# Performance work log

Measured on AMD Instinct MI355X. Metric: run time of the kernel, lower is better.

The kernel has to match this reference:

```python
import jax, jax.numpy as jnp
import numpy as np

N = 1048576          # total points
B = 2048             # number of point clouds (segments)
FEAT = 64            # per-point feature dim
ENC = 32             # neighborhood encoder output dim
RADIUS = 1.0


def _linear_params(key, fan_in, fan_out):
    k1, k2 = jax.random.split(key)
    bound = 1.0 / np.sqrt(fan_in)
    w = jax.random.uniform(k1, (fan_in, fan_out), minval=-bound, maxval=bound, dtype=jnp.float32)
    b = jax.random.uniform(k2, (fan_out,), minval=-bound, maxval=bound, dtype=jnp.float32)
    return w, b


def setup_inputs() -> dict:
    key = jax.random.key(0)
    ks = jax.random.split(key, 10)
    points = jax.random.normal(ks[0], (N, 3), dtype=jnp.float32)
    features = jax.random.normal(ks[1], (N, FEAT), dtype=jnp.float32)
    batch = jnp.sort(jax.random.randint(ks[2], (N,), 0, B)).astype(jnp.int64)
    w_ne, b_ne = _linear_params(ks[3], 3, ENC)
    w1, b1 = _linear_params(ks[4], ENC + FEAT, 128)
    w2, b2 = _linear_params(ks[5], 128, 128)
    w3, b3 = _linear_params(ks[6], 128, 128)
    wg1, bg1 = _linear_params(ks[7], 128, 128)
    wg2, bg2 = _linear_params(ks[8], 128, 64)
    wg3, bg3 = _linear_params(ks[9], 64, 32)
    return {"points": points, "features": features, "batch": batch,
            "w_ne": w_ne, "b_ne": b_ne,
            "w1": w1, "b1": b1, "w2": w2, "b2": b2, "w3": w3, "b3": b3,
            "wg1": wg1, "bg1": bg1, "wg2": wg2, "bg2": bg2, "wg3": wg3, "bg3": bg3}


def _segment_max(x, batch, num_segments):
    pooled = jax.ops.segment_max(x, batch, num_segments=num_segments, indices_are_sorted=True)
    # guard empty segments (segment_max fills with -inf)
    return jnp.where(jnp.isneginf(pooled), 0.0, pooled)


def reference(points, features, batch, w_ne, b_ne, w1, b1, w2, b2, w3, b3,
              wg1, bg1, wg2, bg2, wg3, bg3):
    relative_points = points / RADIUS                       # [N, 3]
    # neighborhood encoder: per-point Linear+ReLU, then segment max-pool -> [B, ENC]
    enc = jax.nn.relu(relative_points @ w_ne + b_ne)        # [N, ENC]
    rel_encoded = _segment_max(enc, batch, B)               # [B, ENC]
    rel_enc_mapped = rel_encoded[batch]                     # gather -> [N, ENC]
    fc_input = jnp.concatenate([rel_enc_mapped, features], axis=1)  # [N, ENC+FEAT]
    h = jax.nn.relu(fc_input @ w1 + b1)                     # [N, 128]
    h = jax.nn.relu(h @ w2 + b2)                            # [N, 128]
    h = jax.nn.relu(h @ w3 + b3)                            # [N, 128]
    pooled = _segment_max(h, batch, B)                      # [B, 128]
    g = jax.nn.relu(pooled @ wg1 + bg1)                     # [B, 128]
    g = jax.nn.relu(g @ wg2 + bg2)                          # [B, 64]
    g = jax.nn.relu(g @ wg3 + bg3)                          # [B, 32]
    return g
```

## Files before the change

### kernel.cpp

```cpp
#include <hip/hip_runtime.h>
#include <hip/hip_fp16.h>

#define N_PTS 1048576
#define BSEG  2048
#define XSTR  72

typedef _Float16 half8  __attribute__((ext_vector_type(8)));
typedef _Float16 half4  __attribute__((ext_vector_type(4)));
typedef _Float16 half2v __attribute__((ext_vector_type(2)));
typedef float    floatx4 __attribute__((ext_vector_type(4)));

__global__ __launch_bounds__(256) void wconv(const float* __restrict__ w1,
                                             const float* __restrict__ w2,
                                             const float* __restrict__ w3,
                                             _Float16* __restrict__ w1T,
                                             _Float16* __restrict__ w2T,
                                             _Float16* __restrict__ w3T) {
    int idx = blockIdx.x * 256 + threadIdx.x;
    if (idx < 8192) {
        int j = idx >> 6, k = idx & 63;
        w1T[idx] = (_Float16)w1[(32 + k) * 128 + j];
    } else if (idx < 8192 + 16384) {
        int i = idx - 8192; int j = i >> 7, k = i & 127;
        w2T[i] = (_Float16)w2[k * 128 + j];
    } else if (idx < 8192 + 32768) {
        int i = idx - 8192 - 16384; int j = i >> 7, k = i & 127;
        w3T[i] = (_Float16)w3[k * 128 + j];
    }
}

__global__ __launch_bounds__(256) void enc_pool(const float* __restrict__ pts,
                                                const int* __restrict__ batch,
                                                const float* __restrict__ wne,
                                                const float* __restrict__ bne,
                                                const float* __restrict__ w1,
                                                const float* __restrict__ b1,
                                                float* __restrict__ b1p) {
    const int b = blockIdx.x, tid = threadIdx.x;
    __shared__ float swne[96];
    __shared__ float sbne[32];
    __shared__ float red[4][32];
    __shared__ float sEnc[32];
    if (tid < 96) swne[tid] = wne[tid];
    if (tid < 32) sbne[tid] = bne[tid];

    int lo = 0, hi = N_PTS;
    while (lo < hi) { int mid = (lo + hi) >> 1; if (batch[mid] < b) lo = mid + 1; else hi = mid; }
    const int start = lo;
    hi = N_PTS;
    while (lo < hi) { int mid = (lo + hi) >> 1; if (batch[mid] < b + 1) lo = mid + 1; else hi = mid; }
    const int end = lo;
    __syncthreads();

    float mx[32];
#pragma unroll
    for (int j = 0; j < 32; j++) mx[j] = 0.f;
    for (int p = start + tid; p < end; p += 256) {
        float x0 = pts[3 * p], x1 = pts[3 * p + 1], x2 = pts[3 * p + 2];
#pragma unroll
        for (int j = 0; j < 32; j++) {
            float e = fmaf(x0, swne[j], fmaf(x1, swne[32 + j], fmaf(x2, swne[64 + j], sbne[j])));
            mx[j] = fmaxf(mx[j], e);
        }
    }
#pragma unroll
    for (int j = 0; j < 32; j++) {
#pragma unroll
        for (int off = 1; off < 64; off <<= 1)
            mx[j] = fmaxf(mx[j], __shfl_xor(mx[j], off, 64));
    }
    const int wv = tid >> 6;
    if ((tid & 63) == 0) {
#pragma unroll
        for (int j = 0; j < 32; j++) red[wv][j] = mx[j];
    }
    __syncthreads();
    if (tid < 32)
        sEnc[tid] = fmaxf(fmaxf(red[0][tid], red[1][tid]), fmaxf(red[2][tid], red[3][tid]));
    __syncthreads();
    if (tid < 128) {
        float acc = b1[tid];
#pragma unroll 8
        for (int k = 0; k < 32; k++) acc = fmaf(sEnc[k], w1[k * 128 + tid], acc);
        b1p[b * 128 + tid] = acc;
    }
}

__global__ __launch_bounds__(256, 4) void fused_mlp(
    const float* __restrict__ feat, const int* __restrict__ batch,
    const float* __restrict__ b1p_g,
    const _Float16* __restrict__ w1T, const _Float16* __restrict__ w2T,
    const _Float16* __restrict__ w3T,
    const float* __restrict__ b2, const float* __restrict__ b3,
    const float* __restrict__ wg1, const float* __restrict__ bg1,
    const float* __restrict__ wg2, const float* __restrict__ bg2,
    const float* __restrict__ wg3, const float* __restrict__ bg3,
    float* __restrict__ out) {
    __shared__ __attribute__((aligned(16))) _Float16 xf[2][16 * XSTR];
    __shared__ __attribute__((aligned(16))) _Float16 h1s[16 * 128];
    __shared__ __attribute__((aligned(16))) _Float16 h2s[16 * 128];
    __shared__ float pooled[128];
    __shared__ float g1s[128];
    __shared__ float g2s[64];

    const int b = blockIdx.x, tid = threadIdx.x;
    const int lane = tid & 63, jq = tid >> 6;
    const int l15 = lane & 15, quad = lane >> 4;
    const int podd = l15 & 1;

    int lo = 0, hi = N_PTS;
    while (lo < hi) { int mid = (lo + hi) >> 1; if (batch[mid] < b) lo = mid + 1; else hi = mid; }
    const int start = lo;
    hi = N_PTS;
    while (lo < hi) { int mid = (lo + hi) >> 1; if (batch[mid] < b + 1) lo = mid + 1; else hi = mid; }
    const int end = lo;
    const int n = end - start;
    const int niter = (n + 15) >> 4;

    if (tid < 128) pooled[tid] = 0.f;

    const int jc0 = jq * 32 + l15, jc1 = jc0 + 16;
    half8 w1f[2][2], w2f[2][4], w3f[2][4];
#pragma unroll
    for (int ks = 0; ks < 2; ks++) {
        w1f[0][ks] = *(const half8*)(w1T + jc0 * 64 + ks * 32 + quad * 8);
        w1f[1][ks] = *(const half8*)(w1T + jc1 * 64 + ks * 32 + quad * 8);
    }
#pragma unroll
    for (int ks = 0; ks < 4; ks++) {
        w2f[0][ks] = *(const half8*)(w2T + jc0 * 128 + ks * 32 + quad * 8);
        w2f[1][ks] = *(const half8*)(w2T + jc1 * 128 + ks * 32 + quad * 8);
        w3f[0][ks] = *(const half8*)(w3T + jc0 * 128 + ks * 32 + quad * 8);
        w3f[1][ks] = *(const half8*)(w3T + jc1 * 128 + ks * 32 + quad * 8);
    }
    float bb1[2], bb2[2], bb3[2];
    bb1[0] = b1p_g[b * 128 + jc0]; bb1[1] = b1p_g[b * 128 + jc1];
    bb2[0] = b2[jc0]; bb2[1] = b2[jc1];
    bb3[0] = b3[jc0]; bb3[1] = b3[jc1];

    const int srow = tid >> 4, scol = tid & 15;
    floatx4 pf;
    auto issue = [&](int it) {
        int p = start + it * 16 + srow;
        if (p < end) pf = *(const floatx4*)(feat + (size_t)p * 64 + scol * 4);
        else         pf = (floatx4){0.f, 0.f, 0.f, 0.f};
    };
    auto commit = [&](int buf) {
        half4 hv = {(_Float16)pf.x, (_Float16)pf.y, (_Float16)pf.z, (_Float16)pf.w};
        *(half4*)(&xf[buf][srow * XSTR + scol * 4]) = hv;
    };
    auto storeH = [&](_Float16* hbuf, floatx4* acc, float* bb) {
#pragma unroll
        for (int jt = 0; jt < 2; jt++) {
            float v0 = fmaxf(acc[jt][0] + bb[jt], 0.f);
            float v1 = fmaxf(acc[jt][1] + bb[jt], 0.f);
            float v2 = fmaxf(acc[jt][2] + bb[jt], 0.f);
            float v3 = fmaxf(acc[jt][3] + bb[jt], 0.f);
            float s0 = podd ? v0 : v2;
            float s1 = podd ? v1 : v3;
            s0 = __shfl_xor(s0, 1, 64);
            s1 = __shfl_xor(s1, 1, 64);
            float lo0 = podd ? s0 : v0, hi0 = podd ? v2 : s0;
            float lo1 = podd ? s1 : v1, hi1 = podd ? v3 : s1;
            int r0 = quad * 4 + (podd ? 2 : 0);
            int c0 = jq * 32 + jt * 16 + (l15 & ~1);
            int off0 = r0 * 128 + ((((c0 >> 3) ^ r0) & 15) << 3) + (c0 & 7);
            int r1 = r0 + 1;
            int off1 = r1 * 128 + ((((c0 >> 3) ^ r1) & 15) << 3) + (c0 & 7);
            *(half2v*)(&hbuf[off0]) = (half2v){(_Float16)lo0, (_Float16)hi0};
            *(half2v*)(&hbuf[off1]) = (half2v){(_Float16)lo1, (_Float16)hi1};
        }
    };

    if (niter > 0) { issue(0); commit(0); if (niter > 1) issue(1); }
    __syncthreads();

    float vmax[2] = {0.f, 0.f};

    for (int it = 0; it < niter; it++) {
        const int buf = it & 1;
        floatx4 acc[2];

        acc[0] = (floatx4){0.f, 0.f, 0.f, 0.f};
        acc[1] = (floatx4){0.f, 0.f, 0.f, 0.f};
#pragma unroll
        for (int ks = 0; ks < 2; ks++) {
            half8 a = *(const half8*)(&xf[buf][l15 * XSTR + ks * 32 + quad * 8]);
            acc[0] = __builtin_amdgcn_mfma_f32_16x16x32_f16(a, w1f[0][ks], acc[0], 0, 0, 0);
            acc[1] = __builtin_amdgcn_mfma_f32_16x16x32_f16(a, w1f[1][ks], acc[1], 0, 0, 0);
        }
        storeH(h1s, acc, bb1);
        __syncthreads();

        acc[0] = (floatx4){0.f, 0.f, 0.f, 0.f};
        acc[1] = (floatx4){0.f, 0.f, 0.f, 0.f};
#pragma unroll
        for (int ks = 0; ks < 4; ks++) {
            half8 a = *(const half8*)(&h1s[(l15 << 7) + ((((ks * 4 + quad) ^ l15) & 15) << 3)]);
            acc[0] = __builtin_amdgcn_mfma_f32_16x16x32_f16(a, w2f[0][ks], acc[0], 0, 0, 0);
            acc[1] = __builtin_amdgcn_mfma_f32_16x16x32_f16(a, w2f[1][ks], acc[1], 0, 0, 0);
        }
        storeH(h2s, acc, bb2);
        if (it + 1 < niter) { commit(buf ^ 1); if (it + 2 < niter) issue(it + 2); }
        __syncthreads();

        acc[0] = (floatx4){0.f, 0.f, 0.f, 0.f};
        acc[1] = (floatx4){0.f, 0.f, 0.f, 0.f};
#pragma unroll
        for (int ks = 0; ks < 4; ks++) {
            half8 a = *(const half8*)(&h2s[(l15 << 7) + ((((ks * 4 + quad) ^ l15) & 15) << 3)]);
            acc[0] = __builtin_amdgcn_mfma_f32_16x16x32_f16(a, w3f[0][ks], acc[0], 0, 0, 0);
            acc[1] = __builtin_amdgcn_mfma_f32_16x16x32_f16(a, w3f[1][ks], acc[1], 0, 0, 0);
        }
        const int rowbase = it * 16 + quad * 4;
#pragma unroll
        for (int jt = 0; jt < 2; jt++) {
#pragma unroll
            for (int r = 0; r < 4; r++) {
                float v = ((rowbase + r) < n) ? fmaxf(acc[jt][r] + bb3[jt], 0.f) : 0.f;
                vmax[jt] = fmaxf(vmax[jt], v);
            }
        }
    }

#pragma unroll
    for (int jt = 0; jt < 2; jt++) {
        float m = vmax[jt];
        m = fmaxf(m, __shfl_xor(m, 16, 64));
        m = fmaxf(m, __shfl_xor(m, 32, 64));
        if (quad == 0) pooled[jq * 32 + jt * 16 + l15] = m;
    }
    __syncthreads();

    if (tid < 128) {
        float acc = bg1[tid];
#pragma unroll 8
        for (int k = 0; k < 128; k++) acc = fmaf(pooled[k], wg1[k * 128 + tid], acc);
        g1s[tid] = fmaxf(acc, 0.f);
    }
    __syncthreads();
    if (tid < 64) {
        float acc = bg2[tid];
#pragma unroll 8
        for (int k = 0; k < 128; k++) acc = fmaf(g1s[k], wg2[k * 64 + tid], acc);
        g2s[tid] = fmaxf(acc, 0.f);
    }
    __syncthreads();
    if (tid < 32) {
        float acc = bg3[tid];
#pragma unroll 8
        for (int k = 0; k < 64; k++) acc = fmaf(g2s[k], wg3[k * 32 + tid], acc);
        out[b * 32 + tid] = fmaxf(acc, 0.f);
    }
}

extern "C" void kernel_launch(void* const* d_in, const int* in_sizes, int n_in,
                              void* d_out, int out_size, void* d_ws, size_t ws_size,
                              hipStream_t stream) {
    const float* points = (const float*)d_in[0];
    const float* feat   = (const float*)d_in[1];
    const int*   batch  = (const int*)d_in[2];
    const float* w_ne   = (const float*)d_in[3];
    const float* b_ne   = (const float*)d_in[4];
    const float* w1  = (const float*)d_in[5];
    const float* b1  = (const float*)d_in[6];
    const float* w2  = (const float*)d_in[7];
    const float* b2  = (const float*)d_in[8];
    const float* w3  = (const float*)d_in[9];
    const float* b3  = (const float*)d_in[10];
    const float* wg1 = (const float*)d_in[11];
    const float* bg1 = (const float*)d_in[12];
    const float* wg2 = (const float*)d_in[13];
    const float* bg2 = (const float*)d_in[14];
    const float* wg3 = (const float*)d_in[15];
    const float* bg3 = (const float*)d_in[16];
    float* out = (float*)d_out;

    char* ws = (char*)d_ws;
    float*    b1p = (float*)ws;
    _Float16* w1T = (_Float16*)(ws + 1048576);
    _Float16* w2T = (_Float16*)(ws + 1048576 + 16384);
    _Float16* w3T = (_Float16*)(ws + 1048576 + 16384 + 32768);

    wconv<<<160, 256, 0, stream>>>(w1, w2, w3, w1T, w2T, w3T);
    enc_pool<<<BSEG, 256, 0, stream>>>(points, batch, w_ne, b_ne, w1, b1, b1p);
    fused_mlp<<<BSEG, 256, 0, stream>>>(feat, batch, b1p, w1T, w2T, w3T,
                                        b2, b3, wg1, bg1, wg2, bg2, wg3, bg3, out);
}
```

Baseline: 554.9 us.

## Fuse encoder pooling into MLP kernel and transpose MFMA operands

Merges the neighborhood encoder max-pool kernel into the fused MLP kernel, so the per-segment layer-1 bias is computed into shared memory and one launch plus the global round-trip is dropped. Swaps the MFMA operand order so each lane holds 4 consecutive output columns. This allows padded-stride half4 stores and vector bias loads, and the bias now initialises the accumulator. It also stops keeping w2/w3 fragments resident in registers and reloads them from global/L2 each iteration to lower register pressure. The cost is extra per-iteration weight loads and the encoder loop now running inside the MLP kernel's occupancy budget.

```diff
diff --git a/kernel.cpp b/kernel.cpp
--- a/kernel.cpp
+++ b/kernel.cpp
@@ -4,10 +4,10 @@
 #define N_PTS 1048576
 #define BSEG  2048
 #define XSTR  72
+#define HSTR  136
 
 typedef _Float16 half8  __attribute__((ext_vector_type(8)));
 typedef _Float16 half4  __attribute__((ext_vector_type(4)));
-typedef _Float16 half2v __attribute__((ext_vector_type(2)));
 typedef float    floatx4 __attribute__((ext_vector_type(4)));
 
 __global__ __launch_bounds__(256) void wconv(const float* __restrict__ w1,
@@ -29,114 +29,98 @@
     }
 }
 
-__global__ __launch_bounds__(256) void enc_pool(const float* __restrict__ pts,
-                                                const int* __restrict__ batch,
-                                                const float* __restrict__ wne,
-                                                const float* __restrict__ bne,
-                                                const float* __restrict__ w1,
-                                                const float* __restrict__ b1,
-                                                float* __restrict__ b1p) {
-    const int b = blockIdx.x, tid = threadIdx.x;
-    __shared__ float swne[96];
-    __shared__ float sbne[32];
-    __shared__ float red[4][32];
-    __shared__ float sEnc[32];
-    if (tid < 96) swne[tid] = wne[tid];
-    if (tid < 32) sbne[tid] = bne[tid];
-
-    int lo = 0, hi = N_PTS;
-    while (lo < hi) { int mid = (lo + hi) >> 1; if (batch[mid] < b) lo = mid + 1; else hi = mid; }
-    const int start = lo;
-    hi = N_PTS;
-    while (lo < hi) { int mid = (lo + hi) >> 1; if (batch[mid] < b + 1) lo = mid + 1; else hi = mid; }
-    const int end = lo;
-    __syncthreads();
-
-    float mx[32];
-#pragma unroll
-    for (int j = 0; j < 32; j++) mx[j] = 0.f;
-    for (int p = start + tid; p < end; p += 256) {
-        float x0 = pts[3 * p], x1 = pts[3 * p + 1], x2 = pts[3 * p + 2];
-#pragma unroll
-        for (int j = 0; j < 32; j++) {
-            float e = fmaf(x0, swne[j], fmaf(x1, swne[32 + j], fmaf(x2, swne[64 + j], sbne[j])));
-            mx[j] = fmaxf(mx[j], e);
-        }
-    }
-#pragma unroll
-    for (int j = 0; j < 32; j++) {
-#pragma unroll
-        for (int off = 1; off < 64; off <<= 1)
-            mx[j] = fmaxf(mx[j], __shfl_xor(mx[j], off, 64));
-    }
-    const int wv = tid >> 6;
-    if ((tid & 63) == 0) {
-#pragma unroll
-        for (int j = 0; j < 32; j++) red[wv][j] = mx[j];
-    }
-    __syncthreads();
-    if (tid < 32)
-        sEnc[tid] = fmaxf(fmaxf(red[0][tid], red[1][tid]), fmaxf(red[2][tid], red[3][tid]));
-    __syncthreads();
-    if (tid < 128) {
-        float acc = b1[tid];
-#pragma unroll 8
-        for (int k = 0; k < 32; k++) acc = fmaf(sEnc[k], w1[k * 128 + tid], acc);
-        b1p[b * 128 + tid] = acc;
-    }
-}
-
-__global__ __launch_bounds__(256, 4) void fused_mlp(
-    const float* __restrict__ feat, const int* __restrict__ batch,
-    const float* __restrict__ b1p_g,
+__global__ __launch_bounds__(256, 4) void fused_all(
+    const float* __restrict__ pts, const float* __restrict__ feat,
+    const int* __restrict__ batch,
+    const float* __restrict__ wne, const float* __restrict__ bne,
+    const float* __restrict__ w1, const float* __restrict__ b1,
     const _Float16* __restrict__ w1T, const _Float16* __restrict__ w2T,
     const _Float16* __restrict__ w3T,
     const float* __restrict__ b2, const float* __restrict__ b3,
     const float* __restrict__ wg1, const float* __restrict__ bg1,
     const float* __restrict__ wg2, const float* __restrict__ bg2,
     const float* __restrict__ wg3, const float* __restrict__ bg3,
-    float* __restrict__ out) {
+    float* __restrict__ out)
+{
     __shared__ __attribute__((aligned(16))) _Float16 xf[2][16 * XSTR];
-    __shared__ __attribute__((aligned(16))) _Float16 h1s[16 * 128];
-    __shared__ __attribute__((aligned(16))) _Float16 h2s[16 * 128];
-    __shared__ float pooled[128];
+    __shared__ __attribute__((aligned(16))) _Float16 h1s[16 * HSTR];
+    __shared__ __attribute__((aligned(16))) _Float16 h2s[16 * HSTR];
+    __shared__ __attribute__((aligned(16))) float b1ps[128];
+    __shared__ __attribute__((aligned(16))) float pooled[128];
     __shared__ float g1s[128];
     __shared__ float g2s[64];
+    __shared__ float swne[96];
+    __shared__ float sbne[32];
+    __shared__ float sEnc[32];
+    __shared__ float red16[16][33];
 
     const int b = blockIdx.x, tid = threadIdx.x;
     const int lane = tid & 63, jq = tid >> 6;
     const int l15 = lane & 15, quad = lane >> 4;
-    const int podd = l15 & 1;
+
+    if (tid < 96) swne[tid] = wne[tid];
+    if (tid < 32) sbne[tid] = bne[tid];
 
     int lo = 0, hi = N_PTS;
     while (lo < hi) { int mid = (lo + hi) >> 1; if (batch[mid] < b) lo = mid + 1; else hi = mid; }
-    const int start = lo;
+    const int start = __builtin_amdgcn_readfirstlane(lo);
     hi = N_PTS;
     while (lo < hi) { int mid = (lo + hi) >> 1; if (batch[mid] < b + 1) lo = mid + 1; else hi = mid; }
-    const int end = lo;
+    const int end = __builtin_amdgcn_readfirstlane(lo);
     const int n = end - start;
     const int niter = (n + 15) >> 4;
-
-    if (tid < 128) pooled[tid] = 0.f;
+    __syncthreads();
+
+    {
+        float mx[32];
+#pragma unroll
+        for (int j = 0; j < 32; j++) mx[j] = 0.f;
+        for (int p = start + tid; p < end; p += 256) {
+            float x0 = pts[3 * p], x1 = pts[3 * p + 1], x2 = pts[3 * p + 2];
+#pragma unroll
+            for (int j = 0; j < 32; j++) {
+                float e = fmaf(x0, swne[j], fmaf(x1, swne[32 + j], fmaf(x2, swne[64 + j], sbne[j])));
+                mx[j] = fmaxf(mx[j], e);
+            }
+        }
+#pragma unroll
+        for (int j = 0; j < 32; j++) {
+#pragma unroll
+            for (int off = 1; off < 16; off <<= 1)
+                mx[j] = fmaxf(mx[j], __shfl_xor(mx[j], off, 64));
+        }
+        if (l15 == 0) {
+            const int qi = tid >> 4;
+#pragma unroll
+            for (int j = 0; j < 32; j++) red16[qi][j] = mx[j];
+        }
+        __syncthreads();
+        if (tid < 32) {
+            float m = red16[0][tid];
+#pragma unroll
+            for (int q = 1; q < 16; q++) m = fmaxf(m, red16[q][tid]);
+            sEnc[tid] = m;
+        }
+        __syncthreads();
+        if (tid < 128) {
+            float acc = b1[tid];
+#pragma unroll 8
+            for (int k = 0; k < 32; k++) acc = fmaf(sEnc[k], w1[k * 128 + tid], acc);
+            b1ps[tid] = acc;
+        }
+    }
 
     const int jc0 = jq * 32 + l15, jc1 = jc0 + 16;
-    half8 w1f[2][2], w2f[2][4], w3f[2][4];
+    half8 w1f[2][2];
 #pragma unroll
     for (int ks = 0; ks < 2; ks++) {
         w1f[0][ks] = *(const half8*)(w1T + jc0 * 64 + ks * 32 + quad * 8);
         w1f[1][ks] = *(const half8*)(w1T + jc1 * 64 + ks * 32 + quad * 8);
     }
-#pragma unroll
-    for (int ks = 0; ks < 4; ks++) {
-        w2f[0][ks] = *(const half8*)(w2T + jc0 * 128 + ks * 32 + quad * 8);
-        w2f[1][ks] = *(const half8*)(w2T + jc1 * 128 + ks * 32 + quad * 8);
-        w3f[0][ks] = *(const half8*)(w3T + jc0 * 128 + ks * 32 + quad * 8);
-        w3f[1][ks] = *(const half8*)(w3T + jc1 * 128 + ks * 32 + quad * 8);
-    }
-    float bb1[2], bb2[2], bb3[2];
-    bb1[0] = b1p_g[b * 128 + jc0]; bb1[1] = b1p_g[b * 128 + jc1];
-    bb2[0] = b2[jc0]; bb2[1] = b2[jc1];
-    bb3[0] = b3[jc0]; bb3[1] = b3[jc1];
+    const int j0 = jq * 32 + quad * 4;
+    floatx4 bb2[2], bb3[2];
+    bb2[0] = *(const floatx4*)(b2 + j0); bb2[1] = *(const floatx4*)(b2 + j0 + 16);
+    bb3[0] = *(const floatx4*)(b3 + j0); bb3[1] = *(const floatx4*)(b3 + j0 + 16);
 
     const int srow = tid >> 4, scol = tid & 15;
     floatx4 pf;
@@ -149,86 +133,89 @@
         half4 hv = {(_Float16)pf.x, (_Float16)pf.y, (_Float16)pf.z, (_Float16)pf.w};
         *(half4*)(&xf[buf][srow * XSTR + scol * 4]) = hv;
     };
-    auto storeH = [&](_Float16* hbuf, floatx4* acc, float* bb) {
+    auto storeH = [&](_Float16* hbuf, floatx4* acc) {
 #pragma unroll
         for (int jt = 0; jt < 2; jt++) {
-            float v0 = fmaxf(acc[jt][0] + bb[jt], 0.f);
-            float v1 = fmaxf(acc[jt][1] + bb[jt], 0.f);
-            float v2 = fmaxf(acc[jt][2] + bb[jt], 0.f);
-            float v3 = fmaxf(acc[jt][3] + bb[jt], 0.f);
-            float s0 = podd ? v0 : v2;
-            float s1 = podd ? v1 : v3;
-            s0 = __shfl_xor(s0, 1, 64);
-            s1 = __shfl_xor(s1, 1, 64);
-            float lo0 = podd ? s0 : v0, hi0 = podd ? v2 : s0;
-            float lo1 = podd ? s1 : v1, hi1 = podd ? v3 : s1;
-            int r0 = quad * 4 + (podd ? 2 : 0);
-            int c0 = jq * 32 + jt * 16 + (l15 & ~1);
-            int off0 = r0 * 128 + ((((c0 >> 3) ^ r0) & 15) << 3) + (c0 & 7);
-            int r1 = r0 + 1;
-            int off1 = r1 * 128 + ((((c0 >> 3) ^ r1) & 15) << 3) + (c0 & 7);
-            *(half2v*)(&hbuf[off0]) = (half2v){(_Float16)lo0, (_Float16)hi0};
-            *(half2v*)(&hbuf[off1]) = (half2v){(_Float16)lo1, (_Float16)hi1};
+            half4 hv = {(_Float16)fmaxf(acc[jt][0], 0.f), (_Float16)fmaxf(acc[jt][1], 0.f),
+                        (_Float16)fmaxf(acc[jt][2], 0.f), (_Float16)fmaxf(acc[jt][3], 0.f)};
+            *(half4*)(&hbuf[l15 * HSTR + jt * 16 + j0]) = hv;
         }
     };
 
     if (niter > 0) { issue(0); commit(0); if (niter > 1) issue(1); }
     __syncthreads();
 
-    float vmax[2] = {0.f, 0.f};
+    floatx4 bb1[2];
+    bb1[0] = *(const floatx4*)(b1ps + j0); bb1[1] = *(const floatx4*)(b1ps + j0 + 16);
+
+    floatx4 vm[2];
+#pragma unroll
+    for (int i = 0; i < 4; i++) { vm[0][i] = 0.f; vm[1][i] = 0.f; }
 
     for (int it = 0; it < niter; it++) {
         const int buf = it & 1;
+        half8 wf[2][4];
+#pragma unroll
+        for (int ks = 0; ks < 4; ks++) {
+            wf[0][ks] = *(const half8*)(w2T + jc0 * 128 + ks * 32 + quad * 8);
+            wf[1][ks] = *(const half8*)(w2T + jc1 * 128 + ks * 32 + quad * 8);
+        }
         floatx4 acc[2];
 
-        acc[0] = (floatx4){0.f, 0.f, 0.f, 0.f};
-        acc[1] = (floatx4){0.f, 0.f, 0.f, 0.f};
+        acc[0] = bb1[0]; acc[1] = bb1[1];
 #pragma unroll
         for (int ks = 0; ks < 2; ks++) {
             half8 a = *(const half8*)(&xf[buf][l15 * XSTR + ks * 32 + quad * 8]);
-            acc[0] = __builtin_amdgcn_mfma_f32_16x16x32_f16(a, w1f[0][ks], acc[0], 0, 0, 0);
-            acc[1] = __builtin_amdgcn_mfma_f32_16x16x32_f16(a, w1f[1][ks], acc[1], 0, 0, 0);
-        }
-        storeH(h1s, acc, bb1);
-        __syncthreads();
-
-        acc[0] = (floatx4){0.f, 0.f, 0.f, 0.f};
-        acc[1] = (floatx4){0.f, 0.f, 0.f, 0.f};
-#pragma unroll
-        for (int ks = 0; ks < 4; ks++) {
-            half8 a = *(const half8*)(&h1s[(l15 << 7) + ((((ks * 4 + quad) ^ l15) & 15) << 3)]);
-            acc[0] = __builtin_amdgcn_mfma_f32_16x16x32_f16(a, w2f[0][ks], acc[0], 0, 0, 0);
-            acc[1] = __builtin_amdgcn_mfma_f32_16x16x32_f16(a, w2f[1][ks], acc[1], 0, 0, 0);
-        }
-        storeH(h2s, acc, bb2);
+            acc[0] = __builtin_amdgcn_mfma_f32_16x16x32_f16(w1f[0][ks], a, acc[0], 0, 0, 0);
+            acc[1] = __builtin_amdgcn_mfma_f32_16x16x32_f16(w1f[1][ks], a, acc[1], 0, 0, 0);
+        }
+        storeH(h1s, acc);
+        __syncthreads();
+
+        acc[0] = bb2[0]; acc[1] = bb2[1];
+#pragma unroll
+        for (int ks = 0; ks < 4; ks++) {
+            half8 a = *(const half8*)(&h1s[l15 * HSTR + ks * 32 + quad * 8]);
+            acc[0] = __builtin_amdgcn_mfma_f32_16x16x32_f16(wf[0][ks], a, acc[0], 0, 0, 0);
+            acc[1] = __builtin_amdgcn_mfma_f32_16x16x32_f16(wf[1][ks], a, acc[1], 0, 0, 0);
+        }
+#pragma unroll
+        for (int ks = 0; ks < 4; ks++) {
+            wf[0][ks] = *(const half8*)(w3T + jc0 * 128 + ks * 32 + quad * 8);
+            wf[1][ks] = *(const half8*)(w3T + jc1 * 128 + ks * 32 + quad * 8);
+        }
+        storeH(h2s, acc);
         if (it + 1 < niter) { commit(buf ^ 1); if (it + 2 < niter) issue(it + 2); }
         __syncthreads();
 
-        acc[0] = (floatx4){0.f, 0.f, 0.f, 0.f};
-        acc[1] = (floatx4){0.f, 0.f, 0.f, 0.f};
-#pragma unroll
-        for (int ks = 0; ks < 4; ks++) {
-            half8 a = *(const half8*)(&h2s[(l15 << 7) + ((((ks * 4 + quad) ^ l15) & 15) << 3)]);
-            acc[0] = __builtin_amdgcn_mfma_f32_16x16x32_f16(a, w3f[0][ks], acc[0], 0, 0, 0);
-            acc[1] = __builtin_amdgcn_mfma_f32_16x16x32_f16(a, w3f[1][ks], acc[1], 0, 0, 0);
-        }
-        const int rowbase = it * 16 + quad * 4;
-#pragma unroll
-        for (int jt = 0; jt < 2; jt++) {
-#pragma unroll
-            for (int r = 0; r < 4; r++) {
-                float v = ((rowbase + r) < n) ? fmaxf(acc[jt][r] + bb3[jt], 0.f) : 0.f;
-                vmax[jt] = fmaxf(vmax[jt], v);
+        acc[0] = bb3[0]; acc[1] = bb3[1];
+#pragma unroll
+        for (int ks = 0; ks < 4; ks++) {
+            half8 a = *(const half8*)(&h2s[l15 * HSTR + ks * 32 + quad * 8]);
+            acc[0] = __builtin_amdgcn_mfma_f32_16x16x32_f16(wf[0][ks], a, acc[0], 0, 0, 0);
+            acc[1] = __builtin_amdgcn_mfma_f32_16x16x32_f16(wf[1][ks], a, acc[1], 0, 0, 0);
+        }
+        if (it * 16 + l15 < n) {
+#pragma unroll
+            for (int i = 0; i < 4; i++) {
+                vm[0][i] = fmaxf(vm[0][i], acc[0][i]);
+                vm[1][i] = fmaxf(vm[1][i], acc[1][i]);
             }
         }
     }
 
 #pragma unroll
     for (int jt = 0; jt < 2; jt++) {
-        float m = vmax[jt];
-        m = fmaxf(m, __shfl_xor(m, 16, 64));
-        m = fmaxf(m, __shfl_xor(m, 32, 64));
-        if (quad == 0) pooled[jq * 32 + jt * 16 + l15] = m;
+#pragma unroll
+        for (int off = 1; off < 16; off <<= 1) {
+#pragma unroll
+            for (int i = 0; i < 4; i++)
+                vm[jt][i] = fmaxf(vm[jt][i], __shfl_xor(vm[jt][i], off, 64));
+        }
+    }
+    if (l15 == 0) {
+        *(floatx4*)(pooled + j0)      = vm[0];
+        *(floatx4*)(pooled + j0 + 16) = vm[1];
     }
     __syncthreads();
 
@@ -277,13 +264,12 @@
     float* out = (float*)d_out;
 
     char* ws = (char*)d_ws;
-    float*    b1p = (float*)ws;
-    _Float16* w1T = (_Float16*)(ws + 1048576);
-    _Float16* w2T = (_Float16*)(ws + 1048576 + 16384);
-    _Float16* w3T = (_Float16*)(ws + 1048576 + 16384 + 32768);
+    _Float16* w1T = (_Float16*)ws;
+    _Float16* w2T = (_Float16*)(ws + 16384);
+    _Float16* w3T = (_Float16*)(ws + 49152);
 
     wconv<<<160, 256, 0, stream>>>(w1, w2, w3, w1T, w2T, w3T);
-    enc_pool<<<BSEG, 256, 0, stream>>>(points, batch, w_ne, b_ne, w1, b1, b1p);
-    fused_mlp<<<BSEG, 256, 0, stream>>>(feat, batch, b1p, w1T, w2T, w3T,
-                                        b2, b3, wg1, bg1, wg2, bg2, wg3, bg3, out);
+    fused_all<<<BSEG, 256, 0, stream>>>(points, feat, batch, w_ne, b_ne, w1, b1,
+                                        w1T, w2T, w3T, b2, b3,
+                                        wg1, bg1, wg2, bg2, wg3, bg3, out);
 }
```

New measurement: 634.6 us. 14.3% more time.
